# Kernel optimization log

Measured on AMD Instinct MI355X. Metric: run time of the kernel, lower is better.

Reference implementation:

```python
import jax, jax.numpy as jnp
import numpy as np

N_NODES = 50000
N_EDGES = 800000
IN_CH, OUT_CH, HEADS = 64, 32, 4
NEG_SLOPE = 0.2
BN_EPS = 1e-5


def setup_inputs() -> dict:
    key = jax.random.key(0)
    ks = jax.random.split(key, 9)
    x = jax.random.normal(ks[0], (N_NODES, IN_CH), dtype=jnp.float32)
    pos = jax.random.uniform(ks[1], (N_NODES, 3), dtype=jnp.float32)
    edge_index = jax.random.randint(ks[2], (2, N_EDGES), 0, N_NODES, dtype=jnp.int64)
    s = 1.0 / np.sqrt(IN_CH)
    W_l = jax.random.normal(ks[3], (IN_CH, HEADS * OUT_CH), dtype=jnp.float32) * s
    W_r = jax.random.normal(ks[4], (IN_CH, HEADS * OUT_CH), dtype=jnp.float32) * s
    W_edge = jax.random.normal(ks[5], (3, HEADS * OUT_CH), dtype=jnp.float32) * 0.5
    att = jax.random.normal(ks[6], (HEADS, OUT_CH), dtype=jnp.float32) * (1.0 / np.sqrt(OUT_CH))
    bn_gamma = jax.random.uniform(ks[7], (HEADS * OUT_CH,), dtype=jnp.float32, minval=0.5, maxval=1.5)
    bn_beta = jax.random.normal(ks[8], (HEADS * OUT_CH,), dtype=jnp.float32) * 0.1
    return {"x": x, "pos": pos, "edge_index": edge_index, "W_l": W_l, "W_r": W_r,
            "W_edge": W_edge, "att": att, "bn_gamma": bn_gamma, "bn_beta": bn_beta}


def reference(x, pos, edge_index, W_l, W_r, W_edge, att, bn_gamma, bn_beta):
    N = x.shape[0]
    H, C = att.shape
    # source->target projections (GATv2: lin_l for source/messages, lin_r for target)
    xl = (x @ W_l).reshape(N, H, C)
    xr = (x @ W_r).reshape(N, H, C)
    src, dst = edge_index[0], edge_index[1]
    edge_attr = pos[src] - pos[dst]  # [E,3] relative position as edge feature
    # add self-loops with fill_value='mean' (PyG default)
    loop = jnp.arange(N)
    src = jnp.concatenate([src, loop])
    dst = jnp.concatenate([dst, loop])
    mean_attr = edge_attr.mean(axis=0, keepdims=True)  # [1,3]
    edge_attr = jnp.concatenate([edge_attr, jnp.broadcast_to(mean_attr, (N, 3))], axis=0)
    # per-edge GATv2 score: att . LeakyReLU(x_l[j] + x_r[i] + W_e e_ij)
    e_feat = (edge_attr @ W_edge).reshape(-1, H, C)
    msg = xl[src]                              # [Et,H,C] (reused for aggregation)
    e = msg + xr[dst] + e_feat
    e = jax.nn.leaky_relu(e, NEG_SLOPE)
    score = jnp.einsum('ehc,hc->eh', e, att)   # [Et,H]
    # segment softmax over destination node
    m = jax.ops.segment_max(score, dst, num_segments=N)
    score = jnp.exp(score - m[dst])
    denom = jax.ops.segment_sum(score, dst, num_segments=N)
    alpha = score / (denom[dst] + 1e-16)       # [Et,H]
    out = jax.ops.segment_sum(alpha[:, :, None] * msg, dst, num_segments=N)
    out = out.reshape(N, H * C)
    # BatchNorm over node dimension (training-mode batch statistics, PyG BatchNorm)
    mu = out.mean(axis=0)
    var = out.var(axis=0)
    return (out - mu) / jnp.sqrt(var + BN_EPS) * bn_gamma + bn_beta
```

## Files before the change

kernel.cpp:

```cpp
#include <hip/hip_runtime.h>
#include <hip/hip_bf16.h>
#include <hip/hip_fp16.h>

#define N_NODES 50000
#define IN_CH 64
#define HC 128
#define CAP 64
#define NEG_SLOPE 0.2f
#define BN_EPS 1e-5f


__global__ __launch_bounds__(256) void k_gemm(const float* __restrict__ x,
                                              const float* __restrict__ Wl,
                                              const float* __restrict__ Wr,
                                              unsigned int* __restrict__ xl_bf,
                                              float* __restrict__ xr_out,
                                              int* __restrict__ deg,
                                              float* __restrict__ mean_sums,
                                              float* __restrict__ bn_sums,
                                              int* __restrict__ flag,
                                              const int* __restrict__ eidx) {
  {
    int gtid = blockIdx.x * 256 + threadIdx.x;
    if (gtid < N_NODES) deg[gtid] = 1;
    if (gtid < 256) bn_sums[gtid] = 0.f;
    if (gtid < 3) mean_sums[gtid] = 0.f;
    if (blockIdx.x == 0 && threadIdx.x < 64) {
      int w = eidx[2 * threadIdx.x + 1];
      unsigned long long nz = __ballot(w != 0);
      if (threadIdx.x == 0) flag[0] = (nz == 0ULL) ? 1 : 0;
    }
  }

  __shared__ float xs[16][IN_CH];
  __shared__ __hip_bfloat162 wsm[IN_CH][128];
  const int t = threadIdx.x;
  const int row0 = blockIdx.x * 16;

  for (int i = 0; i < 32; ++i) {
    int k = i * 2 + (t >> 7);
    int p = t & 127;
    int cc = p * 2;
    float2 wv;
    if (cc < 128) wv = *(const float2*)(Wl + k * 128 + cc);
    else          wv = *(const float2*)(Wr + k * 128 + (cc - 128));
    wsm[k][p] = __float22bfloat162_rn(wv);
  }
  {
    int r = t >> 4, c4 = (t & 15) * 4;
    *(float4*)&xs[r][c4] = *(const float4*)(x + (row0 + r) * IN_CH + c4);
  }
  __syncthreads();

  const int ct = t & 63;
  const int rt = t >> 6;
  const int c4 = ct * 4;
  const int r4 = rt * 4;

  float acc[4][4];
  #pragma unroll
  for (int a = 0; a < 4; ++a)
    #pragma unroll
    for (int b = 0; b < 4; ++b) acc[a][b] = 0.f;

  #pragma unroll 8
  for (int k = 0; k < IN_CH; ++k) {
    uint2 wraw = *(const uint2*)&wsm[k][ct * 2];
    float2 f01 = __bfloat1622float2(*(__hip_bfloat162*)&wraw.x);
    float2 f23 = __bfloat1622float2(*(__hip_bfloat162*)&wraw.y);
    float wv[4] = {f01.x, f01.y, f23.x, f23.y};
    float xv[4] = {xs[r4][k], xs[r4 + 1][k], xs[r4 + 2][k], xs[r4 + 3][k]};
    #pragma unroll
    for (int a = 0; a < 4; ++a)
      #pragma unroll
      for (int b = 0; b < 4; ++b) acc[a][b] = fmaf(xv[a], wv[b], acc[a][b]);
  }

  #pragma unroll
  for (int a = 0; a < 4; ++a) {
    int row = row0 + r4 + a;
    if (c4 < 128) {
      __hip_bfloat162 b01 = __float22bfloat162_rn(make_float2(acc[a][0], acc[a][1]));
      __hip_bfloat162 b23 = __float22bfloat162_rn(make_float2(acc[a][2], acc[a][3]));
      uint2 u;
      u.x = *(unsigned int*)&b01;
      u.y = *(unsigned int*)&b23;
      *(uint2*)(xl_bf + row * 64 + (c4 >> 1)) = u;
    } else {
      float4 v = make_float4(acc[a][0], acc[a][1], acc[a][2], acc[a][3]);
      *(float4*)(xr_out + row * HC + (c4 - 128)) = v;
    }
  }
}

__device__ __forceinline__ uint2 packslot(int s, float dx, float dy, float dz) {
  __half2 hxy = __halves2half2(__float2half_rn(dx), __float2half_rn(dy));
  uint2 r;
  r.x = *(unsigned int*)&hxy;
  r.y = ((unsigned int)s << 16) | (unsigned int)__half_as_ushort(__float2half_rn(dz));
  return r;
}

__global__ __launch_bounds__(256) void k_edges(const int* __restrict__ eidx,
                                               const float* __restrict__ pos,
                                               int* __restrict__ deg,
                                               uint2* __restrict__ bucket,
                                               float* __restrict__ mean_sums,
                                               const int* __restrict__ flag,
                                               int E) {
  const bool w64 = flag[0] != 0;
  const int tid = blockIdx.x * 256 + threadIdx.x;
  const int base = tid * 8;
  float sx = 0.f, sy = 0.f, sz = 0.f;

  const bool vec_ok = w64 ? ((E & 1) == 0) : ((E & 3) == 0);

  if (base + 8 <= E && vec_ok) {
    int s[8], d[8];
    if (w64) {
      const int4* ps = (const int4*)(eidx + 2 * base);
      int4 A = ps[0], B = ps[1], C = ps[2], D = ps[3];
      s[0]=A.x; s[1]=A.z; s[2]=B.x; s[3]=B.z; s[4]=C.x; s[5]=C.z; s[6]=D.x; s[7]=D.z;
      const int4* pd = (const int4*)(eidx + 2 * E + 2 * base);
      A = pd[0]; B = pd[1]; C = pd[2]; D = pd[3];
      d[0]=A.x; d[1]=A.z; d[2]=B.x; d[3]=B.z; d[4]=C.x; d[5]=C.z; d[6]=D.x; d[7]=D.z;
    } else {
      int4 A = *(const int4*)(eidx + base);
      int4 B = *(const int4*)(eidx + base + 4);
      s[0]=A.x; s[1]=A.y; s[2]=A.z; s[3]=A.w; s[4]=B.x; s[5]=B.y; s[6]=B.z; s[7]=B.w;
      A = *(const int4*)(eidx + E + base);
      B = *(const int4*)(eidx + E + base + 4);
      d[0]=A.x; d[1]=A.y; d[2]=A.z; d[3]=A.w; d[4]=B.x; d[5]=B.y; d[6]=B.z; d[7]=B.w;
    }
    int slot[8];
    #pragma unroll
    for (int k = 0; k < 8; ++k) slot[k] = atomicAdd(&deg[d[k]], 1);
    float dx[8], dy[8], dz[8];
    #pragma unroll
    for (int k = 0; k < 8; ++k) {
      dx[k] = pos[3 * s[k]]     - pos[3 * d[k]];
      dy[k] = pos[3 * s[k] + 1] - pos[3 * d[k] + 1];
      dz[k] = pos[3 * s[k] + 2] - pos[3 * d[k] + 2];
      sx += dx[k]; sy += dy[k]; sz += dz[k];
    }
    #pragma unroll
    for (int k = 0; k < 8; ++k)
      if (slot[k] < CAP) bucket[d[k] * CAP + slot[k]] = packslot(s[k], dx[k], dy[k], dz[k]);
  } else if (base < E) {
    int hi = min(base + 8, E);
    for (int e = base; e < hi; ++e) {
      int s, d;
      if (w64) { s = eidx[2 * e]; d = eidx[2 * (E + e)]; }
      else     { s = eidx[e];     d = eidx[E + e]; }
      int o = atomicAdd(&deg[d], 1);
      float dx = pos[3 * s]     - pos[3 * d];
      float dy = pos[3 * s + 1] - pos[3 * d + 1];
      float dz = pos[3 * s + 2] - pos[3 * d + 2];
      sx += dx; sy += dy; sz += dz;
      if (o < CAP) bucket[d * CAP + o] = packslot(s, dx, dy, dz);
    }
  }

  #pragma unroll
  for (int m = 1; m < 64; m <<= 1) {
    sx += __shfl_xor(sx, m); sy += __shfl_xor(sy, m); sz += __shfl_xor(sz, m);
  }
  __shared__ float red[4][3];
  int wave = threadIdx.x >> 6, lane = threadIdx.x & 63;
  if (lane == 0) { red[wave][0] = sx; red[wave][1] = sy; red[wave][2] = sz; }
  __syncthreads();
  if (threadIdx.x == 0) {
    float a = 0.f, b = 0.f, c = 0.f;
    for (int w = 0; w < 4; ++w) { a += red[w][0]; b += red[w][1]; c += red[w][2]; }
    unsafeAtomicAdd(&mean_sums[0], a);
    unsafeAtomicAdd(&mean_sums[1], b);
    unsafeAtomicAdd(&mean_sums[2], c);
  }
}

__device__ __forceinline__ void edge4(int s, float dx, float dy, float dz, bool valid,
                                      const unsigned int* __restrict__ xl_bf, int l5,
                                      float4 xr4, float4 at4, float4 w0, float4 w1, float4 w2,
                                      float& a0, float& a1, float& a2, float& a3, float& den) {
  uint2 raw = *(const uint2*)(xl_bf + (s << 6) + (l5 << 1));
  float2 x01 = __bfloat1622float2(*(__hip_bfloat162*)&raw.x);
  float2 x23 = __bfloat1622float2(*(__hip_bfloat162*)&raw.y);
  float t0 = x01.x + xr4.x; t0 = fmaf(dx, w0.x, t0); t0 = fmaf(dy, w1.x, t0); t0 = fmaf(dz, w2.x, t0);
  float t1 = x01.y + xr4.y; t1 = fmaf(dx, w0.y, t1); t1 = fmaf(dy, w1.y, t1); t1 = fmaf(dz, w2.y, t1);
  float t2 = x23.x + xr4.z; t2 = fmaf(dx, w0.z, t2); t2 = fmaf(dy, w1.z, t2); t2 = fmaf(dz, w2.z, t2);
  float t3 = x23.y + xr4.w; t3 = fmaf(dx, w0.w, t3); t3 = fmaf(dy, w1.w, t3); t3 = fmaf(dz, w2.w, t3);
  float l0 = fmaxf(t0, NEG_SLOPE * t0);
  float l1 = fmaxf(t1, NEG_SLOPE * t1);
  float l2 = fmaxf(t2, NEG_SLOPE * t2);
  float l3 = fmaxf(t3, NEG_SLOPE * t3);
  float sc = l0 * at4.x;
  sc = fmaf(l1, at4.y, sc); sc = fmaf(l2, at4.z, sc); sc = fmaf(l3, at4.w, sc);
  sc += __shfl_xor(sc, 1); sc += __shfl_xor(sc, 2); sc += __shfl_xor(sc, 4);
  float e = __expf(sc);
  float p = valid ? e : 0.f;
  den += p;
  a0 = fmaf(p, x01.x, a0); a1 = fmaf(p, x01.y, a1);
  a2 = fmaf(p, x23.x, a2); a3 = fmaf(p, x23.y, a3);
}

__global__ __launch_bounds__(256) void k_agg(const unsigned int* __restrict__ xl_bf,
                                             float* __restrict__ xr_out,
                                             const float* __restrict__ att,
                                             const float* __restrict__ We,
                                             const float* __restrict__ mean_sums,
                                             const uint2* __restrict__ bucket,
                                             const int* __restrict__ deg,
                                             float invE,
                                             float* __restrict__ bn_sums) {
  __shared__ __align__(16) float redS[4][128];
  __shared__ __align__(16) float redQ[4][128];
  const int lane = threadIdx.x & 63;
  const int half = lane >> 5;
  const int l5 = lane & 31;
  const int c = l5 << 2;
  const int wave = threadIdx.x >> 6;

  const float4 at4 = *(const float4*)(att + c);
  const float4 w0 = *(const float4*)(We + c);
  const float4 w1 = *(const float4*)(We + 128 + c);
  const float4 w2 = *(const float4*)(We + 256 + c);
  const float m0 = mean_sums[0] * invE;
  const float m1 = mean_sums[1] * invE;
  const float m2 = mean_sums[2] * invE;

  const int gw = blockIdx.x * 4 + wave;
  const int W = gridDim.x * 4;

  float4 bs = make_float4(0.f, 0.f, 0.f, 0.f);
  float4 bq = make_float4(0.f, 0.f, 0.f, 0.f);

  for (int i = gw; i < N_NODES; i += W) {
    const float4 xr4 = *(const float4*)(xr_out + i * HC + c);
    const int di = min(deg[i], CAP);
    uint2 se = make_uint2(0u, 0u);
    if (lane < di) se = bucket[i * CAP + lane];
    float a0 = 0.f, a1 = 0.f, a2 = 0.f, a3 = 0.f, den = 0.f;

    {
      const int jB = 2 + half;
      uint2 wA, wB;
      wA.x = (unsigned)__shfl((int)se.x, 1);  wA.y = (unsigned)__shfl((int)se.y, 1);
      wB.x = (unsigned)__shfl((int)se.x, jB); wB.y = (unsigned)__shfl((int)se.y, jB);
      float2 dA = __half22float2(*(__half2*)&wA.x);
      float dzA = __half2float(__ushort_as_half((unsigned short)(wA.y & 0xffffu)));
      int sA = (int)(wA.y >> 16);
      if (half == 0) { sA = i; dA.x = m0; dA.y = m1; dzA = m2; }
      const bool vA = half < di;
      if (!vA) sA = i;
      float2 dB = __half22float2(*(__half2*)&wB.x);
      float dzB = __half2float(__ushort_as_half((unsigned short)(wB.y & 0xffffu)));
      int sB = (int)(wB.y >> 16);
      const bool vB = jB < di;
      if (!vB) sB = i;
      edge4(sA, dA.x, dA.y, dzA, vA, xl_bf, l5, xr4, at4, w0, w1, w2, a0, a1, a2, a3, den);
      edge4(sB, dB.x, dB.y, dzB, vB, xl_bf, l5, xr4, at4, w0, w1, w2, a0, a1, a2, a3, den);
    }

    for (int j = 4; j < di; j += 4) {
      const int jA = j + half;
      const int jB = j + 2 + half;
      uint2 wA, wB;
      wA.x = (unsigned)__shfl((int)se.x, jA); wA.y = (unsigned)__shfl((int)se.y, jA);
      wB.x = (unsigned)__shfl((int)se.x, jB); wB.y = (unsigned)__shfl((int)se.y, jB);
      float2 dA = __half22float2(*(__half2*)&wA.x);
      float dzA = __half2float(__ushort_as_half((unsigned short)(wA.y & 0xffffu)));
      int sA = (int)(wA.y >> 16);
      const bool vA = jA < di;
      if (!vA) sA = i;
      float2 dB = __half22float2(*(__half2*)&wB.x);
      float dzB = __half2float(__ushort_as_half((unsigned short)(wB.y & 0xffffu)));
      int sB = (int)(wB.y >> 16);
      const bool vB = jB < di;
      if (!vB) sB = i;
      edge4(sA, dA.x, dA.y, dzA, vA, xl_bf, l5, xr4, at4, w0, w1, w2, a0, a1, a2, a3, den);
      edge4(sB, dB.x, dB.y, dzB, vB, xl_bf, l5, xr4, at4, w0, w1, w2, a0, a1, a2, a3, den);
    }

    den += __shfl_xor(den, 32);
    a0 += __shfl_xor(a0, 32);
    a1 += __shfl_xor(a1, 32);
    a2 += __shfl_xor(a2, 32);
    a3 += __shfl_xor(a3, 32);

    const float inv = 1.f / (den + 1e-16f);
    if (half == 0) {
      float4 o = make_float4(a0 * inv, a1 * inv, a2 * inv, a3 * inv);
      *(float4*)(xr_out + i * HC + c) = o;
      bs.x += o.x; bs.y += o.y; bs.z += o.z; bs.w += o.w;
      bq.x = fmaf(o.x, o.x, bq.x); bq.y = fmaf(o.y, o.y, bq.y);
      bq.z = fmaf(o.z, o.z, bq.z); bq.w = fmaf(o.w, o.w, bq.w);
    }
  }

  if (half == 0) {
    *(float4*)&redS[wave][c] = bs;
    *(float4*)&redQ[wave][c] = bq;
  }
  __syncthreads();
  const int t = threadIdx.x;
  if (t < 128) {
    float s = redS[0][t] + redS[1][t] + redS[2][t] + redS[3][t];
    float q = redQ[0][t] + redQ[1][t] + redQ[2][t] + redQ[3][t];
    unsafeAtomicAdd(&bn_sums[t], s);
    unsafeAtomicAdd(&bn_sums[128 + t], q);
  }
}

__global__ __launch_bounds__(256) void k_bnapply(float* __restrict__ out,
                                                 const float* __restrict__ bn_sums,
                                                 const float* __restrict__ gamma,
                                                 const float* __restrict__ beta,
                                                 int n4) {
  const int stride = gridDim.x * blockDim.x;
  const float invN = 1.f / (float)N_NODES;
  for (int i = blockIdx.x * blockDim.x + threadIdx.x; i < n4; i += stride) {
    int c = (i & 31) * 4;
    float4 v = ((float4*)out)[i];
    float4 s = *(const float4*)(bn_sums + c);
    float4 q = *(const float4*)(bn_sums + 128 + c);
    float4 g = *(const float4*)(gamma + c);
    float4 b = *(const float4*)(beta + c);
    float mu, var, rstd;
    mu = s.x * invN; var = q.x * invN - mu * mu; rstd = rsqrtf(var + BN_EPS);
    v.x = (v.x - mu) * rstd * g.x + b.x;
    mu = s.y * invN; var = q.y * invN - mu * mu; rstd = rsqrtf(var + BN_EPS);
    v.y = (v.y - mu) * rstd * g.y + b.y;
    mu = s.z * invN; var = q.z * invN - mu * mu; rstd = rsqrtf(var + BN_EPS);
    v.z = (v.z - mu) * rstd * g.z + b.z;
    mu = s.w * invN; var = q.w * invN - mu * mu; rstd = rsqrtf(var + BN_EPS);
    v.w = (v.w - mu) * rstd * g.w + b.w;
    ((float4*)out)[i] = v;
  }
}

extern "C" void kernel_launch(void* const* d_in, const int* in_sizes, int n_in,
                              void* d_out, int out_size, void* d_ws, size_t ws_size,
                              hipStream_t stream) {
  const float* x     = (const float*)d_in[0];
  const float* pos   = (const float*)d_in[1];
  const int*   eidx  = (const int*)d_in[2];
  const float* Wl    = (const float*)d_in[3];
  const float* Wr    = (const float*)d_in[4];
  const float* We    = (const float*)d_in[5];
  const float* att   = (const float*)d_in[6];
  const float* gamma = (const float*)d_in[7];
  const float* beta  = (const float*)d_in[8];
  float* out = (float*)d_out;
  const int E = in_sizes[2] / 2;

  char* ws = (char*)d_ws;
  int*   flag      = (int*)(ws + 0);
  float* mean_sums = (float*)(ws + 64);
  float* bn_sums   = (float*)(ws + 1024);
  int*   deg       = (int*)(ws + 4096);
  uint2* bucket    = (uint2*)(ws + (1 << 19));
  unsigned int* xl_bf = (unsigned int*)(ws + (1 << 19) + (size_t)N_NODES * CAP * 8);

  k_gemm<<<N_NODES / 16, 256, 0, stream>>>(x, Wl, Wr, xl_bf, out,
                                           deg, mean_sums, bn_sums, flag, eidx);
  int eblocks = (E + 2047) / 2048;
  k_edges<<<eblocks, 256, 0, stream>>>(eidx, pos, deg, bucket, mean_sums, flag, E);
  k_agg<<<2048, 256, 0, stream>>>(xl_bf, out, att, We, mean_sums, bucket, deg,
                                  1.f / (float)E, bn_sums);
  k_bnapply<<<512, 256, 0, stream>>>(out, bn_sums, gamma, beta, out_size / 4);
}
```

Measured before the change: 251.5 us.

## Software-pipeline edge gathers and prefetch next node bucket via LDS double buffer

The aggregation kernel now prefetches the next node's edge bucket into registers and stages it in a per-wave double-buffered LDS row. It also software-pipelines the xl gather loads one iteration ahead of the score/softmax compute, and replaces the shfl_xor reduction over 8 lanes with DPP moves. The goal is to hide the latency of the dependent bucket-to-xl gather chain and to cut cross-lane shuffle cost. In exchange, register pressure rises and LDS use grows. The LDS reads of slots 64-71 past the filled entries return stale data, which is masked by the validity flag.

```diff
diff --git a/kernel.cpp b/kernel.cpp
--- a/kernel.cpp
+++ b/kernel.cpp
@@ -178,11 +178,17 @@
   }
 }
 
-__device__ __forceinline__ void edge4(int s, float dx, float dy, float dz, bool valid,
-                                      const unsigned int* __restrict__ xl_bf, int l5,
-                                      float4 xr4, float4 at4, float4 w0, float4 w1, float4 w2,
-                                      float& a0, float& a1, float& a2, float& a3, float& den) {
-  uint2 raw = *(const uint2*)(xl_bf + (s << 6) + (l5 << 1));
+__device__ __forceinline__ float sum8_dpp(float v) {
+  v += __int_as_float(__builtin_amdgcn_mov_dpp(__float_as_int(v), 0xB1, 0xF, 0xF, true));
+  v += __int_as_float(__builtin_amdgcn_mov_dpp(__float_as_int(v), 0x4E, 0xF, 0xF, true));
+  v += __int_as_float(__builtin_amdgcn_mov_dpp(__float_as_int(v), 0x141, 0xF, 0xF, true));
+  return v;
+}
+
+__device__ __forceinline__ void edge_compute(uint2 raw, float dx, float dy, float dz, bool valid,
+                                             const float4& xr4, const float4& at4,
+                                             const float4& w0, const float4& w1, const float4& w2,
+                                             float& a0, float& a1, float& a2, float& a3, float& den) {
   float2 x01 = __bfloat1622float2(*(__hip_bfloat162*)&raw.x);
   float2 x23 = __bfloat1622float2(*(__hip_bfloat162*)&raw.y);
   float t0 = x01.x + xr4.x; t0 = fmaf(dx, w0.x, t0); t0 = fmaf(dy, w1.x, t0); t0 = fmaf(dz, w2.x, t0);
@@ -195,12 +201,22 @@
   float l3 = fmaxf(t3, NEG_SLOPE * t3);
   float sc = l0 * at4.x;
   sc = fmaf(l1, at4.y, sc); sc = fmaf(l2, at4.z, sc); sc = fmaf(l3, at4.w, sc);
-  sc += __shfl_xor(sc, 1); sc += __shfl_xor(sc, 2); sc += __shfl_xor(sc, 4);
+  sc = sum8_dpp(sc);
   float e = __expf(sc);
   float p = valid ? e : 0.f;
   den += p;
   a0 = fmaf(p, x01.x, a0); a1 = fmaf(p, x01.y, a1);
   a2 = fmaf(p, x23.x, a2); a3 = fmaf(p, x23.y, a3);
+}
+
+__device__ __forceinline__ void slotNZ(const uint2* __restrict__ row, int j, int di, int i,
+                                       int& s, float& dx, float& dy, float& dz, bool& v) {
+  uint2 w = row[j];
+  v = j < di;
+  s = v ? (int)(w.y >> 16) : i;
+  float2 dd = __half22float2(*(__half2*)&w.x);
+  dx = dd.x; dy = dd.y;
+  dz = __half2float(__ushort_as_half((unsigned short)(w.y & 0xffffu)));
 }
 
 __global__ __launch_bounds__(256) void k_agg(const unsigned int* __restrict__ xl_bf,
@@ -212,8 +228,10 @@
                                              const int* __restrict__ deg,
                                              float invE,
                                              float* __restrict__ bn_sums) {
+  __shared__ uint2 rowbuf[4][2][72];
   __shared__ __align__(16) float redS[4][128];
   __shared__ __align__(16) float redQ[4][128];
+
   const int lane = threadIdx.x & 63;
   const int half = lane >> 5;
   const int l5 = lane & 31;
@@ -234,52 +252,53 @@
   float4 bs = make_float4(0.f, 0.f, 0.f, 0.f);
   float4 bq = make_float4(0.f, 0.f, 0.f, 0.f);
 
+  int dcur = min(deg[gw], CAP);
+  if (lane < dcur) rowbuf[wave][0][lane] = bucket[gw * CAP + lane];
+  int r = 0;
+
   for (int i = gw; i < N_NODES; i += W) {
+    const int inext = i + W;
+    int dnext = 0;
+    uint2 sregN = make_uint2(0u, 0u);
+    if (inext < N_NODES) {
+      dnext = min(deg[inext], CAP);
+      if (lane < dnext) sregN = bucket[inext * CAP + lane];
+    }
+
+    const uint2* row = rowbuf[wave][r];
     const float4 xr4 = *(const float4*)(xr_out + i * HC + c);
-    const int di = min(deg[i], CAP);
-    uint2 se = make_uint2(0u, 0u);
-    if (lane < di) se = bucket[i * CAP + lane];
+    const int di = dcur;
+
+    int sA, sB;
+    float dxA, dyA, dzA, dxB, dyB, dzB;
+    bool vA, vB;
+    if (half == 0) { sA = i; dxA = m0; dyA = m1; dzA = m2; vA = true; }
+    else           { slotNZ(row, 1, di, i, sA, dxA, dyA, dzA, vA); }
+    slotNZ(row, 2 + half, di, i, sB, dxB, dyB, dzB, vB);
+    uint2 rawA = *(const uint2*)(xl_bf + (sA << 6) + (l5 << 1));
+    uint2 rawB = *(const uint2*)(xl_bf + (sB << 6) + (l5 << 1));
+
     float a0 = 0.f, a1 = 0.f, a2 = 0.f, a3 = 0.f, den = 0.f;
 
-    {
-      const int jB = 2 + half;
-      uint2 wA, wB;
-      wA.x = (unsigned)__shfl((int)se.x, 1);  wA.y = (unsigned)__shfl((int)se.y, 1);
-      wB.x = (unsigned)__shfl((int)se.x, jB); wB.y = (unsigned)__shfl((int)se.y, jB);
-      float2 dA = __half22float2(*(__half2*)&wA.x);
-      float dzA = __half2float(__ushort_as_half((unsigned short)(wA.y & 0xffffu)));
-      int sA = (int)(wA.y >> 16);
-      if (half == 0) { sA = i; dA.x = m0; dA.y = m1; dzA = m2; }
-      const bool vA = half < di;
-      if (!vA) sA = i;
-      float2 dB = __half22float2(*(__half2*)&wB.x);
-      float dzB = __half2float(__ushort_as_half((unsigned short)(wB.y & 0xffffu)));
-      int sB = (int)(wB.y >> 16);
-      const bool vB = jB < di;
-      if (!vB) sB = i;
-      edge4(sA, dA.x, dA.y, dzA, vA, xl_bf, l5, xr4, at4, w0, w1, w2, a0, a1, a2, a3, den);
-      edge4(sB, dB.x, dB.y, dzB, vB, xl_bf, l5, xr4, at4, w0, w1, w2, a0, a1, a2, a3, den);
-    }
-
     for (int j = 4; j < di; j += 4) {
-      const int jA = j + half;
-      const int jB = j + 2 + half;
-      uint2 wA, wB;
-      wA.x = (unsigned)__shfl((int)se.x, jA); wA.y = (unsigned)__shfl((int)se.y, jA);
-      wB.x = (unsigned)__shfl((int)se.x, jB); wB.y = (unsigned)__shfl((int)se.y, jB);
-      float2 dA = __half22float2(*(__half2*)&wA.x);
-      float dzA = __half2float(__ushort_as_half((unsigned short)(wA.y & 0xffffu)));
-      int sA = (int)(wA.y >> 16);
-      const bool vA = jA < di;
-      if (!vA) sA = i;
-      float2 dB = __half22float2(*(__half2*)&wB.x);
-      float dzB = __half2float(__ushort_as_half((unsigned short)(wB.y & 0xffffu)));
-      int sB = (int)(wB.y >> 16);
-      const bool vB = jB < di;
-      if (!vB) sB = i;
-      edge4(sA, dA.x, dA.y, dzA, vA, xl_bf, l5, xr4, at4, w0, w1, w2, a0, a1, a2, a3, den);
-      edge4(sB, dB.x, dB.y, dzB, vB, xl_bf, l5, xr4, at4, w0, w1, w2, a0, a1, a2, a3, den);
-    }
+      int sAn, sBn;
+      float dxAn, dyAn, dzAn, dxBn, dyBn, dzBn;
+      bool vAn, vBn;
+      slotNZ(row, j + half,     di, i, sAn, dxAn, dyAn, dzAn, vAn);
+      slotNZ(row, j + 2 + half, di, i, sBn, dxBn, dyBn, dzBn, vBn);
+      uint2 rawAn = *(const uint2*)(xl_bf + (sAn << 6) + (l5 << 1));
+      uint2 rawBn = *(const uint2*)(xl_bf + (sBn << 6) + (l5 << 1));
+
+      edge_compute(rawA, dxA, dyA, dzA, vA, xr4, at4, w0, w1, w2, a0, a1, a2, a3, den);
+      edge_compute(rawB, dxB, dyB, dzB, vB, xr4, at4, w0, w1, w2, a0, a1, a2, a3, den);
+
+      rawA = rawAn; dxA = dxAn; dyA = dyAn; dzA = dzAn; vA = vAn;
+      rawB = rawBn; dxB = dxBn; dyB = dyBn; dzB = dzBn; vB = vBn;
+    }
+    edge_compute(rawA, dxA, dyA, dzA, vA, xr4, at4, w0, w1, w2, a0, a1, a2, a3, den);
+    edge_compute(rawB, dxB, dyB, dzB, vB, xr4, at4, w0, w1, w2, a0, a1, a2, a3, den);
+
+    if (lane < dnext) rowbuf[wave][r ^ 1][lane] = sregN;
 
     den += __shfl_xor(den, 32);
     a0 += __shfl_xor(a0, 32);
@@ -295,6 +314,8 @@
       bq.x = fmaf(o.x, o.x, bq.x); bq.y = fmaf(o.y, o.y, bq.y);
       bq.z = fmaf(o.z, o.z, bq.z); bq.w = fmaf(o.w, o.w, bq.w);
     }
+
+    dcur = dnext; r ^= 1;
   }
 
   if (half == 0) {
```

Result: faster. 243.9 us (-3.0%).
